# Performance work log

Hardware: AMD Instinct MI355X
Metric: run time of the kernel (lower is better)

Reference implementation:

```python
import jax, jax.numpy as jnp
import numpy as np

TEMPERATURE = 0.5
NEG_FILL = -9000000000000000.0


def setup_inputs() -> dict:
    key = jax.random.key(0)
    z = jax.random.normal(key, (16384, 128), dtype=jnp.float32)
    return {"z": z}


def reference(z) -> jnp.ndarray:
    n2 = z.shape[0]  # 2N
    # L2 normalize rows (eps matches torch F.normalize default 1e-12)
    norm = jnp.maximum(jnp.linalg.norm(z, axis=1, keepdims=True), 1e-12)
    zn = z / norm
    # (2N, 2N) cosine similarity scaled by temperature
    sim = jnp.matmul(zn, zn.T) / TEMPERATURE
    # mask self-similarity on the diagonal
    idx = jnp.arange(n2)
    sim = jnp.where(idx[:, None] == idx[None, :], NEG_FILL, sim)
    # positive pair of row i is i^1 (2i <-> 2i+1)
    pos_indices = idx ^ 1
    pos_sim = sim[idx, pos_indices]
    loss = -pos_sim + jax.scipy.special.logsumexp(sim, axis=1)
    return jnp.mean(loss)
```

## Files before the change

### kernel.cpp

```cpp
#include <hip/hip_runtime.h>
#include <hip/hip_bf16.h>

#define N2 16384
#define D  128
#define PANEL 32768
#define HALFP 16384
#define SQC1 1.69864360258810896f
#define LN2  0.69314718055994530942f

typedef __bf16 bf16x8 __attribute__((ext_vector_type(8)));
typedef float  f32x4  __attribute__((ext_vector_type(4)));

#if __has_builtin(__builtin_amdgcn_exp2f)
#define EXP2(x) __builtin_amdgcn_exp2f(x)
#else
#define EXP2(x) exp2f(x)
#endif

__device__ __forceinline__ unsigned short f2bf(float f) {
    union { float f; unsigned u; } v; v.f = f;
    unsigned r = v.u + 0x7fffu + ((v.u >> 16) & 1u);
    return (unsigned short)(r >> 16);
}

__device__ __forceinline__ void stage_panel(const char* __restrict__ g,
                                            char* lds, int tid) {
    const int wid = tid >> 6, lane = tid & 63;
    #pragma unroll
    for (int i = 0; i < 8; ++i) {
        int off = (wid << 13) + (i << 10) + (lane << 4);
        int src = off ^ (((off >> 8) & 7) << 4);
        __builtin_amdgcn_global_load_lds(
            (const __attribute__((address_space(1))) unsigned*)(g + src),
            (__attribute__((address_space(3))) unsigned*)(lds + (wid << 13) + (i << 10)),
            16, 0, 0);
    }
}

__device__ __forceinline__ void stage_half(const char* __restrict__ g,
                                           char* lds, int tid) {
    const int wid = tid >> 6, lane = tid & 63;
    #pragma unroll
    for (int i = 0; i < 4; ++i) {
        int off = (wid << 12) + (i << 10) + (lane << 4);
        int src = off ^ (((off >> 8) & 7) << 4);
        __builtin_amdgcn_global_load_lds(
            (const __attribute__((address_space(1))) unsigned*)(g + src),
            (__attribute__((address_space(3))) unsigned*)(lds + (wid << 12) + (i << 10)),
            16, 0, 0);
    }
}

__global__ void k_norm(const float* __restrict__ z, unsigned short* __restrict__ zn,
                       float* __restrict__ rowsum, float* __restrict__ out) {
    if (blockIdx.x < 64) rowsum[blockIdx.x * 256 + threadIdx.x] = 0.f;
    if (blockIdx.x == 64 && threadIdx.x == 0) out[0] = 0.f;
    int row  = blockIdx.x * 4 + (threadIdx.x >> 6);
    int lane = threadIdx.x & 63;
    const float2 v = ((const float2*)(z + (size_t)row * D))[lane];
    float ss = v.x * v.x + v.y * v.y;
    #pragma unroll
    for (int m = 1; m < 64; m <<= 1) ss += __shfl_xor(ss, m);
    float inv = SQC1 / fmaxf(sqrtf(ss), 1e-12f);
    ushort2 o; o.x = f2bf(v.x * inv); o.y = f2bf(v.y * inv);
    ((ushort2*)(zn + (size_t)row * D))[lane] = o;
}

__global__ __launch_bounds__(256, 3)
void k_sim(const unsigned short* __restrict__ zn, float* __restrict__ rowsum) {
    __shared__ char ls[PANEL];
    char* ls0 = ls;
    char* ls1 = ls + HALFP;
    const int tileI = blockIdx.y;
    const int c = blockIdx.x;
    const int sLo = c * 11;
    const int sHi = (c < 5) ? (sLo + 11) : ((tileI < 64) ? 65 : 64);
    const int Q = (sHi - sLo) * 2;

    const int tid  = threadIdx.x;
    const int lane = tid & 63, wid = tid >> 6;
    const int wr = wid >> 1, wc = wid & 1;
    const int l16 = lane & 15, lg = lane >> 4;
    const char* znb = (const char*)zn;
    const f32x4 ZERO = {0.f, 0.f, 0.f, 0.f};

    stage_panel(znb + (size_t)tileI * PANEL, ls0, tid);
    asm volatile("s_waitcnt vmcnt(0)" ::: "memory");
    __builtin_amdgcn_s_barrier();

    bf16x8 af[4][4];
    #pragma unroll
    for (int kk = 0; kk < 4; ++kk)
        #pragma unroll
        for (int m = 0; m < 4; ++m) {
            int row = wr * 64 + m * 16 + l16;
            int d = row * 256 + kk * 64 + lg * 16;
            af[kk][m] = *(const bf16x8*)(ls0 + (d ^ ((row & 7) << 4)));
        }
    asm volatile("s_waitcnt lgkmcnt(0)" ::: "memory");
    __builtin_amdgcn_s_barrier();

    stage_half(znb + (size_t)((tileI + sLo) & 127) * PANEL, ls0, tid);

    float rs[4][4];
    #pragma unroll
    for (int m = 0; m < 4; ++m)
        #pragma unroll
        for (int r = 0; r < 4; ++r) rs[m][r] = 0.f;

    for (int q = 0; q < Q; ++q) {
        const int s  = sLo + (q >> 1);
        const int h  = q & 1;
        const int jt = (tileI + s) & 127;
        char* rbuf = (q & 1) ? ls1 : ls0;
        char* sbuf = (q & 1) ? ls0 : ls1;
        if (q + 1 < Q) {
            const int s1 = sLo + ((q + 1) >> 1);
            const int h1 = (q + 1) & 1;
            stage_half(znb + (size_t)((tileI + s1) & 127) * PANEL + h1 * HALFP,
                       sbuf, tid);
            asm volatile("s_waitcnt vmcnt(4)" ::: "memory");
        } else {
            asm volatile("s_waitcnt vmcnt(0)" ::: "memory");
        }
        __builtin_amdgcn_s_barrier();

        bf16x8 bfr[4][2];
        #pragma unroll
        for (int kk = 0; kk < 4; ++kk)
            #pragma unroll
            for (int n = 0; n < 2; ++n) {
                int row = wc * 32 + n * 16 + l16;
                int d = row * 256 + kk * 64 + lg * 16;
                bfr[kk][n] = *(const bf16x8*)(rbuf + (d ^ ((row & 7) << 4)));
            }
        asm volatile("s_waitcnt lgkmcnt(0)" ::: "memory");
        __builtin_amdgcn_s_barrier();

        f32x4 acc[4][2];
        #pragma unroll
        for (int m = 0; m < 4; ++m)
            #pragma unroll
            for (int n = 0; n < 2; ++n)
                acc[m][n] = __builtin_amdgcn_mfma_f32_16x16x32_bf16(af[0][m], bfr[0][n], ZERO, 0, 0, 0);
        #pragma unroll
        for (int kk = 1; kk < 4; ++kk)
            #pragma unroll
            for (int m = 0; m < 4; ++m)
                #pragma unroll
                for (int n = 0; n < 2; ++n)
                    acc[m][n] = __builtin_amdgcn_mfma_f32_16x16x32_bf16(af[kk][m], bfr[kk][n], acc[m][n], 0, 0, 0);

        if (s == 0) {
            #pragma unroll
            for (int m = 0; m < 4; ++m)
                #pragma unroll
                for (int r = 0; r < 4; ++r) {
                    int li = wr * 64 + m * 16 + lg * 4 + r;
                    float a = 0.f;
                    #pragma unroll
                    for (int n = 0; n < 2; ++n) {
                        int lj = h * 64 + wc * 32 + n * 16 + l16;
                        float e = EXP2(acc[m][n][r]);
                        a += (li == lj) ? 0.f : e;
                    }
                    rs[m][r] += a;
                }
        } else {
            float cs0 = 0.f, cs1 = 0.f;
            #pragma unroll
            for (int m = 0; m < 4; ++m)
                #pragma unroll
                for (int r = 0; r < 4; ++r) {
                    float e0 = EXP2(acc[m][0][r]);
                    float e1 = EXP2(acc[m][1][r]);
                    rs[m][r] += e0 + e1;
                    cs0 += e0; cs1 += e1;
                }
            float v0 = cs0 + __shfl_xor(cs0, 16);
            v0 += __shfl_xor(v0, 32);
            float v1 = cs1 + __shfl_xor(cs1, 16);
            v1 += __shfl_xor(v1, 32);
            if (lg == 0) {
                atomicAdd(&rowsum[jt * 128 + h * 64 + wc * 32 + l16], v0);
                atomicAdd(&rowsum[jt * 128 + h * 64 + wc * 32 + 16 + l16], v1);
            }
        }
    }

    #pragma unroll
    for (int m = 0; m < 4; ++m)
        #pragma unroll
        for (int r = 0; r < 4; ++r) {
            float v = rs[m][r];
            v += __shfl_xor(v, 1);
            v += __shfl_xor(v, 2);
            v += __shfl_xor(v, 4);
            v += __shfl_xor(v, 8);
            if (l16 == 0)
                atomicAdd(&rowsum[tileI * 128 + wr * 64 + m * 16 + lg * 4 + r], v);
        }
}

__global__ void k_loss_reduce(const unsigned short* __restrict__ zn,
                              const float* __restrict__ rowsum,
                              float* __restrict__ out) {
    const int tid = threadIdx.x + blockIdx.x * 256;
    float p = 0.f;
    const bf16x8* v8 = (const bf16x8*)zn;
    for (int v = tid; v < N2 * D / 8; v += 64 * 256) {
        bf16x8 a = v8[v];
        bf16x8 b = v8[v ^ 16];
        #pragma unroll
        for (int e = 0; e < 8; ++e) p += (float)a[e] * (float)b[e];
    }
    float part = logf(rowsum[tid]) - LN2 * p;

    __shared__ float sm[4];
    #pragma unroll
    for (int m = 1; m < 64; m <<= 1) part += __shfl_xor(part, m);
    if ((threadIdx.x & 63) == 0) sm[threadIdx.x >> 6] = part;
    __syncthreads();
    if (threadIdx.x == 0)
        atomicAdd(out, (sm[0] + sm[1] + sm[2] + sm[3]) * (1.0f / (float)N2));
}

extern "C" void kernel_launch(void* const* d_in, const int* in_sizes, int n_in,
                              void* d_out, int out_size, void* d_ws, size_t ws_size,
                              hipStream_t stream) {
    const float* z = (const float*)d_in[0];
    float* out = (float*)d_out;

    unsigned short* zn = (unsigned short*)d_ws;
    float* rowsum = (float*)((char*)d_ws + (size_t)N2 * D * 2);

    k_norm<<<N2 / 4 , 256, 0, stream>>>(z, zn, rowsum, out);
    dim3 grid(6, 128);
    k_sim<<<grid, 256, 0, stream>>>(zn, rowsum);
    k_loss_reduce<<<64, 256, 0, stream>>>(zn, rowsum, out);
}
```

Baseline: 69.89 us.

## Restructure k_sim pipeline: single barrier per step, deferred column atomics, interleaved B loads

The main loop now uses one barrier per half-panel step instead of two. The prefetch of the next half-panel is issued after that barrier, and the B fragments are loaded per k-slice, interleaved with the MFMAs rather than all loaded up front. Column-sum atomics are deferred by one iteration and issued at the start of the next step, so their latency overlaps the matrix work. The aim is to cut barrier stalls and load-to-use latency in the inner loop. The risks are a tighter vmcnt accounting and a subtle correctness dependency: the deferred atomic must skip the diagonal tile, which is handled by zeroing the pending sums.

```diff
diff --git a/kernel.cpp b/kernel.cpp
--- a/kernel.cpp
+++ b/kernel.cpp
@@ -4,7 +4,7 @@
 #define N2 16384
 #define D  128
 #define PANEL 32768
-#define HALFP 16384
+#define HPAN  16384
 #define SQC1 1.69864360258810896f
 #define LN2  0.69314718055994530942f
 
@@ -23,8 +23,8 @@
     return (unsigned short)(r >> 16);
 }
 
-__device__ __forceinline__ void stage_panel(const char* __restrict__ g,
-                                            char* lds, int tid) {
+__device__ __forceinline__ void stage32(const char* __restrict__ g,
+                                        char* lds, int tid) {
     const int wid = tid >> 6, lane = tid & 63;
     #pragma unroll
     for (int i = 0; i < 8; ++i) {
@@ -37,8 +37,8 @@
     }
 }
 
-__device__ __forceinline__ void stage_half(const char* __restrict__ g,
-                                           char* lds, int tid) {
+__device__ __forceinline__ void stage16(const char* __restrict__ g,
+                                        char* lds, int tid) {
     const int wid = tid >> 6, lane = tid & 63;
     #pragma unroll
     for (int i = 0; i < 4; ++i) {
@@ -70,12 +70,13 @@
 void k_sim(const unsigned short* __restrict__ zn, float* __restrict__ rowsum) {
     __shared__ char ls[PANEL];
     char* ls0 = ls;
-    char* ls1 = ls + HALFP;
+    char* ls1 = ls + HPAN;
+
     const int tileI = blockIdx.y;
     const int c = blockIdx.x;
     const int sLo = c * 11;
-    const int sHi = (c < 5) ? (sLo + 11) : ((tileI < 64) ? 65 : 64);
-    const int Q = (sHi - sLo) * 2;
+    const int ntile = (c < 5) ? 11 : ((tileI < 64) ? 10 : 9);
+    const int nq = ntile * 2;
 
     const int tid  = threadIdx.x;
     const int lane = tid & 63, wid = tid >> 6;
@@ -84,7 +85,7 @@
     const char* znb = (const char*)zn;
     const f32x4 ZERO = {0.f, 0.f, 0.f, 0.f};
 
-    stage_panel(znb + (size_t)tileI * PANEL, ls0, tid);
+    stage32(znb + (size_t)tileI * PANEL, ls, tid);
     asm volatile("s_waitcnt vmcnt(0)" ::: "memory");
     __builtin_amdgcn_s_barrier();
 
@@ -95,61 +96,60 @@
         for (int m = 0; m < 4; ++m) {
             int row = wr * 64 + m * 16 + l16;
             int d = row * 256 + kk * 64 + lg * 16;
-            af[kk][m] = *(const bf16x8*)(ls0 + (d ^ ((row & 7) << 4)));
+            af[kk][m] = *(const bf16x8*)(ls + (d ^ ((row & 7) << 4)));
         }
     asm volatile("s_waitcnt lgkmcnt(0)" ::: "memory");
     __builtin_amdgcn_s_barrier();
 
-    stage_half(znb + (size_t)((tileI + sLo) & 127) * PANEL, ls0, tid);
+    stage16(znb + (size_t)((tileI + sLo) & 127) * PANEL, ls0, tid);
 
     float rs[4][4];
     #pragma unroll
     for (int m = 0; m < 4; ++m)
         #pragma unroll
         for (int r = 0; r < 4; ++r) rs[m][r] = 0.f;
-
-    for (int q = 0; q < Q; ++q) {
+    float csp0 = 0.f, csp1 = 0.f;
+    int jcp = tileI * 128 + wc * 32;
+
+    for (int q = 0; q < nq; ++q) {
         const int s  = sLo + (q >> 1);
         const int h  = q & 1;
         const int jt = (tileI + s) & 127;
         char* rbuf = (q & 1) ? ls1 : ls0;
         char* sbuf = (q & 1) ? ls0 : ls1;
-        if (q + 1 < Q) {
+
+        if (q) { asm volatile("s_waitcnt vmcnt(2)" ::: "memory"); }
+        else   { asm volatile("s_waitcnt vmcnt(0)" ::: "memory"); }
+        __builtin_amdgcn_s_barrier();
+
+        if (q + 1 < nq) {
             const int s1 = sLo + ((q + 1) >> 1);
             const int h1 = (q + 1) & 1;
-            stage_half(znb + (size_t)((tileI + s1) & 127) * PANEL + h1 * HALFP,
-                       sbuf, tid);
-            asm volatile("s_waitcnt vmcnt(4)" ::: "memory");
-        } else {
-            asm volatile("s_waitcnt vmcnt(0)" ::: "memory");
-        }
-        __builtin_amdgcn_s_barrier();
-
-        bf16x8 bfr[4][2];
-        #pragma unroll
-        for (int kk = 0; kk < 4; ++kk)
+            stage16(znb + (size_t)((tileI + s1) & 127) * PANEL + h1 * HPAN,
+                    sbuf, tid);
+        }
+        if (lg == 0) {
+            atomicAdd(&rowsum[jcp + l16], csp0);
+            atomicAdd(&rowsum[jcp + 16 + l16], csp1);
+        }
+
+        f32x4 acc[4][2];
+        bf16x8 bfr[2];
+        #pragma unroll
+        for (int kk = 0; kk < 4; ++kk) {
             #pragma unroll
             for (int n = 0; n < 2; ++n) {
                 int row = wc * 32 + n * 16 + l16;
                 int d = row * 256 + kk * 64 + lg * 16;
-                bfr[kk][n] = *(const bf16x8*)(rbuf + (d ^ ((row & 7) << 4)));
+                bfr[n] = *(const bf16x8*)(rbuf + (d ^ ((row & 7) << 4)));
             }
-        asm volatile("s_waitcnt lgkmcnt(0)" ::: "memory");
-        __builtin_amdgcn_s_barrier();
-
-        f32x4 acc[4][2];
-        #pragma unroll
-        for (int m = 0; m < 4; ++m)
-            #pragma unroll
-            for (int n = 0; n < 2; ++n)
-                acc[m][n] = __builtin_amdgcn_mfma_f32_16x16x32_bf16(af[0][m], bfr[0][n], ZERO, 0, 0, 0);
-        #pragma unroll
-        for (int kk = 1; kk < 4; ++kk)
             #pragma unroll
             for (int m = 0; m < 4; ++m)
                 #pragma unroll
                 for (int n = 0; n < 2; ++n)
-                    acc[m][n] = __builtin_amdgcn_mfma_f32_16x16x32_bf16(af[kk][m], bfr[kk][n], acc[m][n], 0, 0, 0);
+                    acc[m][n] = __builtin_amdgcn_mfma_f32_16x16x32_bf16(
+                        af[kk][m], bfr[n], (kk == 0) ? ZERO : acc[m][n], 0, 0, 0);
+        }
 
         if (s == 0) {
             #pragma unroll
@@ -166,6 +166,8 @@
                     }
                     rs[m][r] += a;
                 }
+            csp0 = csp1 = 0.f;
+            jcp = jt * 128 + h * 64 + wc * 32;
         } else {
             float cs0 = 0.f, cs1 = 0.f;
             #pragma unroll
@@ -177,17 +179,17 @@
                     rs[m][r] += e0 + e1;
                     cs0 += e0; cs1 += e1;
                 }
-            float v0 = cs0 + __shfl_xor(cs0, 16);
-            v0 += __shfl_xor(v0, 32);
-            float v1 = cs1 + __shfl_xor(cs1, 16);
-            v1 += __shfl_xor(v1, 32);
-            if (lg == 0) {
-                atomicAdd(&rowsum[jt * 128 + h * 64 + wc * 32 + l16], v0);
-                atomicAdd(&rowsum[jt * 128 + h * 64 + wc * 32 + 16 + l16], v1);
-            }
-        }
-    }
-
+            cs0 += __shfl_xor(cs0, 16); cs0 += __shfl_xor(cs0, 32);
+            cs1 += __shfl_xor(cs1, 16); cs1 += __shfl_xor(cs1, 32);
+            csp0 = cs0; csp1 = cs1;
+            jcp = jt * 128 + h * 64 + wc * 32;
+        }
+    }
+
+    if (lg == 0) {
+        atomicAdd(&rowsum[jcp + l16], csp0);
+        atomicAdd(&rowsum[jcp + 16 + l16], csp1);
+    }
     #pragma unroll
     for (int m = 0; m < 4; ++m)
         #pragma unroll
@@ -234,7 +236,7 @@
     unsigned short* zn = (unsigned short*)d_ws;
     float* rowsum = (float*)((char*)d_ws + (size_t)N2 * D * 2);
 
-    k_norm<<<N2 / 4 , 256, 0, stream>>>(z, zn, rowsum, out);
+    k_norm<<<N2 / 4, 256, 0, stream>>>(z, zn, rowsum, out);
     dim3 grid(6, 128);
     k_sim<<<grid, 256, 0, stream>>>(zn, rowsum);
     k_loss_reduce<<<64, 256, 0, stream>>>(zn, rowsum, out);
```

New measurement: 68.30 us. -2.3%, faster.
